# Kernel optimization log

Measured on AMD Instinct MI355X. Metric: run time of the kernel, lower is better.

The kernel has to match this reference:

```python
import jax, jax.numpy as jnp
import numpy as np

DIM = 1024
HEADS = 16
HEAD_DIM = DIM // HEADS  # 64


def get_rope_matrix(seq_len: int, dim: int) -> jnp.ndarray:
    # rope[s, d] = concat(cos(s * inv_freq), sin(s * inv_freq))  -> (seq_len, dim)
    half = dim // 2
    inv_freq = 1.0 / (10000.0 ** (jnp.arange(half, dtype=jnp.float32) / half))
    sinusoid = jnp.arange(seq_len, dtype=jnp.float32)[:, None] * inv_freq[None, :]
    return jnp.concatenate([jnp.cos(sinusoid), jnp.sin(sinusoid)], axis=-1)


def setup_inputs() -> dict:
    key = jax.random.key(0)
    ks = jax.random.split(key, 6)
    B, T, D = 2, 2048, DIM
    scale = 1.0 / np.sqrt(D)
    return {
        "x": jax.random.normal(ks[0], (B, T, D), dtype=jnp.float32),
        "Wq": jax.random.normal(ks[1], (D, D), dtype=jnp.float32) * scale,
        "Wk": jax.random.normal(ks[2], (D, D), dtype=jnp.float32) * scale,
        "Wv": jax.random.normal(ks[3], (D, D), dtype=jnp.float32) * scale,
        "Wo": jax.random.normal(ks[4], (D, D), dtype=jnp.float32) * scale,
        "bo": jax.random.normal(ks[5], (D,), dtype=jnp.float32) * 0.01,
    }


def reference(x, Wq, Wk, Wv, Wo, bo):
    B, T, D = x.shape
    H, hd = HEADS, HEAD_DIM

    # projections -> (B, H, T, hd)
    def split_heads(y):
        return y.reshape(B, T, H, hd).transpose(0, 2, 1, 3)

    q = split_heads(x @ Wq)
    k = split_heads(x @ Wk)
    v = split_heads(x @ Wv)

    rope = get_rope_matrix(T, hd)  # (T, hd)

    # apply_rope(v, rope): einsum('...nd,sd->...ns') contracts head_dim -> (B,H,T,T)
    v_r = jnp.einsum('bhnd,sd->bhns', v, rope)

    scores = jax.nn.softmax(jnp.einsum('bhnd,bhmd->bhnm', q, k) / jnp.sqrt(jnp.float32(hd)), axis=-1)
    out = jnp.einsum('bhnm,bhms->bhns', scores, v_r)  # (B,H,T,T)

    # apply_rope(out, rope.T): out2[...,n,s] = sum_t out[...,n,t] * rope[t,s] -> (B,H,T,hd)
    out = jnp.einsum('bhnt,ts->bhns', out, rope)

    out = out.transpose(0, 2, 1, 3).reshape(B, T, D)
    return out @ Wo + bo
```

## Files before the change

kernel.cpp:

```cpp
#include <hip/hip_runtime.h>
#include <math.h>

#define DIM 1024
#define NH 16
#define HD 64
#define TT 2048
#define NTOK 4096

typedef __bf16 bf8v __attribute__((ext_vector_type(8)));
typedef float f4v __attribute__((ext_vector_type(4)));
typedef unsigned short us8 __attribute__((ext_vector_type(8)));
typedef unsigned short us4 __attribute__((ext_vector_type(4)));

static __device__ __forceinline__ unsigned short f2bf(float f) {
    unsigned int u = __float_as_uint(f);
    u += 0x7FFFu + ((u >> 16) & 1u);
    return (unsigned short)(u >> 16);
}
static __device__ __forceinline__ bf8v ld8(const unsigned short* p) {
    return __builtin_bit_cast(bf8v, *(const us8*)p);
}
static __device__ __forceinline__ void gl_lds(const unsigned short* g, unsigned short* l) {
    __builtin_amdgcn_global_load_lds((const __attribute__((address_space(1))) unsigned int*)(g),
                                     (__attribute__((address_space(3))) unsigned int*)(l), 16, 0, 0);
}

__global__ void k_prep(const float* __restrict__ x, unsigned short* __restrict__ xb,
                       const float* __restrict__ Wq, const float* __restrict__ Wk,
                       const float* __restrict__ Wv, unsigned short* __restrict__ wt,
                       float* __restrict__ rope) {
    int tid = threadIdx.x;
    int bb = blockIdx.x;
    if (bb < 4096) {
        int i = bb * 256 + tid;
        float4 v = ((const float4*)x)[i];
        us4 o;
        o[0] = f2bf(v.x); o[1] = f2bf(v.y); o[2] = f2bf(v.z); o[3] = f2bf(v.w);
        *(us4*)&xb[i * 4] = o;
    } else if (bb < 7168) {
        __shared__ float tile[32][33];
        bb -= 4096;
        int z = bb >> 10, rem = bb & 1023;
        int bx = rem & 31, by = rem >> 5;
        const float* W = (z == 0) ? Wq : ((z == 1) ? Wk : Wv);
        int tx = tid & 31, ty = tid >> 5;
        int c0 = bx * 32, k0 = by * 32;
#pragma unroll
        for (int j = 0; j < 4; j++)
            tile[ty + j * 8][tx] = W[(k0 + ty + j * 8) * DIM + c0 + tx];
        __syncthreads();
        unsigned short* out = wt + z * DIM * DIM;
#pragma unroll
        for (int j = 0; j < 4; j++)
            out[(c0 + ty + j * 8) * DIM + k0 + tx] = f2bf(tile[tx][ty + j * 8]);
    } else {
        int i = (bb - 7168) * 256 + tid;
        int s = i >> 6, d = i & 63;
        float inv = exp2f(-(float)(d & 31) * (13.287712379549449f / 32.0f));
        float a = (float)s * inv;
        rope[i] = (d < 32) ? cosf(a) : sinf(a);
    }
}

__global__ void k_R(const float* __restrict__ rope, float* __restrict__ R) {
    __shared__ float red[256];
    int d = blockIdx.x;
    int e = threadIdx.x & 63, sl = threadIdx.x >> 6;
    const float* rp = rope + sl * 512 * 64;
    float acc = 0.f;
    for (int s = 0; s < 512; s++)
        acc += rp[s * 64 + d] * rp[s * 64 + e];
    red[threadIdx.x] = acc;
    __syncthreads();
    if (sl == 0)
        R[d * 64 + e] = (red[e] + red[e + 64]) + (red[e + 128] + red[e + 192]);
}

__global__ void k_wo2(const float* __restrict__ Wo, const float* __restrict__ R,
                      unsigned short* __restrict__ wo2t) {
    __shared__ float Ws[64 * 65];
    __shared__ float Rt[64 * 65];
    int tid = threadIdx.x;
    int h = blockIdx.y, j0 = blockIdx.x * 64;
    for (int idx = tid; idx < 4096; idx += 256) {
        int e = idx >> 6, j = idx & 63;
        Ws[e * 65 + j] = Wo[(h * 64 + e) * DIM + j0 + j];
        Rt[e * 65 + j] = R[j * 64 + e];
    }
    __syncthreads();
    int d = tid & 63, jb = (tid >> 6) * 16;
    float acc[16] = {};
    for (int e = 0; e < 64; e++) {
        float r = Rt[e * 65 + d];
#pragma unroll
        for (int jj = 0; jj < 16; jj++)
            acc[jj] += r * Ws[e * 65 + jb + jj];
    }
#pragma unroll
    for (int jj = 0; jj < 16; jj++)
        wo2t[(j0 + jb + jj) * DIM + h * 64 + d] = f2bf(acc[jj]);
}


__global__ __launch_bounds__(256, 3) void k_gemm_qkv(const unsigned short* __restrict__ A,
                                                     const unsigned short* __restrict__ Bt,
                                                     unsigned short* __restrict__ qk,
                                                     unsigned short* __restrict__ vt) {
    __shared__ unsigned short As[128 * 32];
    __shared__ unsigned short Bs[128 * 32];
    const int K = 1024;
    int tid = threadIdx.x;
    int lane = tid & 63, w = tid >> 6;
    int quad = lane >> 4, l16 = lane & 15;
    int m0 = blockIdx.y * 128, n0 = blockIdx.x * 128;
    int wm = (w >> 1) * 64, wn = (w & 1) * 64;

    int s0 = tid, s1 = 256 + tid;
    int r0 = s0 >> 2, cc0 = ((s0 & 3) ^ (r0 & 3)) * 8;
    int r1 = s1 >> 2, cc1 = ((s1 & 3) ^ (r1 & 3)) * 8;
    const unsigned short* Ag0 = A + (m0 + r0) * K + cc0;
    const unsigned short* Ag1 = A + (m0 + r1) * K + cc1;
    const unsigned short* Bg0 = Bt + (n0 + r0) * K + cc0;
    const unsigned short* Bg1 = Bt + (n0 + r1) * K + cc1;
    int qx = quad ^ (l16 & 3);

    f4v acc[4][4] = {};
    for (int k0 = 0; k0 < K; k0 += 32) {
        __syncthreads();
        gl_lds(Ag0 + k0, &As[s0 * 8]);
        gl_lds(Ag1 + k0, &As[s1 * 8]);
        gl_lds(Bg0 + k0, &Bs[s0 * 8]);
        gl_lds(Bg1 + k0, &Bs[s1 * 8]);
        __syncthreads();
        bf8v af[4], bf[4];
#pragma unroll
        for (int mt = 0; mt < 4; mt++)
            af[mt] = ld8(&As[(wm + mt * 16 + l16) * 32 + qx * 8]);
#pragma unroll
        for (int nt = 0; nt < 4; nt++)
            bf[nt] = ld8(&Bs[(wn + nt * 16 + l16) * 32 + qx * 8]);
#pragma unroll
        for (int mt = 0; mt < 4; mt++)
#pragma unroll
            for (int nt = 0; nt < 4; nt++)
                acc[mt][nt] = __builtin_amdgcn_mfma_f32_16x16x32_bf16(af[mt], bf[nt], acc[mt][nt], 0, 0, 0);
    }
#pragma unroll
    for (int mt = 0; mt < 4; mt++) {
#pragma unroll
        for (int nt = 0; nt < 4; nt++) {
            int gc = n0 + wn + nt * 16 + l16;
            int h = (gc >> 6) & 15;
            int d = gc & 63;
            if (gc < 2048) {
                float qs = (gc < 1024) ? 0.18033688011111793f : 1.0f;
                int mtx = gc >> 10;
                unsigned short* base = qk + mtx * (NTOK * DIM);
#pragma unroll
                for (int r = 0; r < 4; r++) {
                    int gm = m0 + wm + mt * 16 + quad * 4 + r;
                    int b = gm >> 11, t = gm & 2047;
                    base[((b * NH + h) * TT + t) * HD + d] = f2bf(acc[mt][nt][r] * qs);
                }
            } else {
                int gm0 = m0 + wm + mt * 16 + quad * 4;
                int b = gm0 >> 11, t = gm0 & 2047;
                us4 ov;
#pragma unroll
                for (int r = 0; r < 4; r++)
                    ov[r] = f2bf(acc[mt][nt][r]);
                *(us4*)&vt[(((b * NH + h) * HD) + d) * TT + t] = ov;
            }
        }
    }
}

__global__ __launch_bounds__(256, 3) void k_gemm_out(const unsigned short* __restrict__ A,
                                                     const unsigned short* __restrict__ Bt,
                                                     const float* __restrict__ bo,
                                                     float* __restrict__ out) {
    __shared__ unsigned short As[128 * 32];
    __shared__ unsigned short Bs[128 * 32];
    const int K = 1024;
    int tid = threadIdx.x;
    int lane = tid & 63, w = tid >> 6;
    int quad = lane >> 4, l16 = lane & 15;
    int m0 = blockIdx.y * 128, n0 = blockIdx.x * 128;
    int wm = (w >> 1) * 64, wn = (w & 1) * 64;

    int s0 = tid, s1 = 256 + tid;
    int r0 = s0 >> 2, cc0 = ((s0 & 3) ^ (r0 & 3)) * 8;
    int r1 = s1 >> 2, cc1 = ((s1 & 3) ^ (r1 & 3)) * 8;
    const unsigned short* Ag0 = A + (m0 + r0) * K + cc0;
    const unsigned short* Ag1 = A + (m0 + r1) * K + cc1;
    const unsigned short* Bg0 = Bt + (n0 + r0) * K + cc0;
    const unsigned short* Bg1 = Bt + (n0 + r1) * K + cc1;
    int qx = quad ^ (l16 & 3);

    f4v acc[4][4] = {};
    for (int k0 = 0; k0 < K; k0 += 32) {
        __syncthreads();
        gl_lds(Ag0 + k0, &As[s0 * 8]);
        gl_lds(Ag1 + k0, &As[s1 * 8]);
        gl_lds(Bg0 + k0, &Bs[s0 * 8]);
        gl_lds(Bg1 + k0, &Bs[s1 * 8]);
        __syncthreads();
        bf8v af[4], bf[4];
#pragma unroll
        for (int mt = 0; mt < 4; mt++)
            af[mt] = ld8(&As[(wm + mt * 16 + l16) * 32 + qx * 8]);
#pragma unroll
        for (int nt = 0; nt < 4; nt++)
            bf[nt] = ld8(&Bs[(wn + nt * 16 + l16) * 32 + qx * 8]);
#pragma unroll
        for (int mt = 0; mt < 4; mt++)
#pragma unroll
            for (int nt = 0; nt < 4; nt++)
                acc[mt][nt] = __builtin_amdgcn_mfma_f32_16x16x32_bf16(af[mt], bf[nt], acc[mt][nt], 0, 0, 0);
    }
#pragma unroll
    for (int mt = 0; mt < 4; mt++) {
#pragma unroll
        for (int nt = 0; nt < 4; nt++) {
            int gc = n0 + wn + nt * 16 + l16;
            float bias = bo[gc];
#pragma unroll
            for (int r = 0; r < 4; r++) {
                int gm = m0 + wm + mt * 16 + quad * 4 + r;
                out[gm * DIM + gc] = acc[mt][nt][r] + bias;
            }
        }
    }
}

#define LQ 72
__global__ __launch_bounds__(256, 4) void k_flash(const unsigned short* __restrict__ qk,
                                                  const unsigned short* __restrict__ vt,
                                                  unsigned short* __restrict__ Op,
                                                  float* __restrict__ Ls) {
    __shared__ unsigned short Ks[64 * LQ];
    __shared__ unsigned short Vs[80 * LQ];
    __shared__ unsigned short Ps[128 * LQ];
    int tid = threadIdx.x;
    int lane = tid & 63, w = tid >> 6;
    int quad = lane >> 4, l16 = lane & 15;
    int bh = blockIdx.x & 31;
    int sp = (blockIdx.x >> 5) & 1;
    int qt = blockIdx.x >> 6;
    const unsigned short* Qg = qk + bh * (TT * HD);
    const unsigned short* Kg = qk + NTOK * DIM + bh * (TT * HD);
    const unsigned short* Vtg = vt + bh * (HD * TT);

    for (int idx = tid; idx < 16 * LQ; idx += 256)
        Vs[64 * LQ + idx] = (idx < LQ) ? (unsigned short)0x3F80 : (unsigned short)0;

    {
        int r = tid >> 1, c0 = (tid & 1) * 32;
        const us8* src = (const us8*)(Qg + (qt * 128 + r) * HD + c0);
#pragma unroll
        for (int i = 0; i < 4; i++)
            *(us8*)&Ps[r * LQ + c0 + i * 8] = src[i];
    }
    bf8v qf[2][2];
#pragma unroll
    for (int g = 0; g < 2; g++)
#pragma unroll
        for (int ks = 0; ks < 2; ks++)
            qf[g][ks] = ld8(&Ps[(w * 32 + g * 16 + l16) * LQ + ks * 32 + quad * 8]);

    int sr = tid >> 2, sc = (tid & 3) * 16;
    const unsigned short* Kgp = Kg + (sp * 1024 + sr) * HD + sc;
    const unsigned short* Vgp = Vtg + sr * TT + sp * 1024 + sc;
    us8 kr0 = *(const us8*)(Kgp);
    us8 kr1 = *(const us8*)(Kgp + 8);
    us8 vr0 = *(const us8*)(Vgp);
    us8 vr1 = *(const us8*)(Vgp + 8);

    f4v oacc[5][2] = {};

    for (int it = 0; it < 16; it++) {
        __syncthreads();
        *(us8*)&Ks[sr * LQ + sc] = kr0;
        *(us8*)&Ks[sr * LQ + sc + 8] = kr1;
        *(us8*)&Vs[sr * LQ + sc] = vr0;
        *(us8*)&Vs[sr * LQ + sc + 8] = vr1;
        __syncthreads();
        if (it < 15) {
            Kgp += 64 * HD;
            Vgp += 64;
            kr0 = *(const us8*)(Kgp);
            kr1 = *(const us8*)(Kgp + 8);
            vr0 = *(const us8*)(Vgp);
            vr1 = *(const us8*)(Vgp + 8);
        }

        f4v sacc[4][2] = {};
#pragma unroll
        for (int ks = 0; ks < 2; ks++) {
            bf8v kf[4];
#pragma unroll
            for (int mt = 0; mt < 4; mt++)
                kf[mt] = ld8(&Ks[(mt * 16 + l16) * LQ + ks * 32 + quad * 8]);
#pragma unroll
            for (int mt = 0; mt < 4; mt++)
#pragma unroll
                for (int g = 0; g < 2; g++)
                    sacc[mt][g] = __builtin_amdgcn_mfma_f32_16x16x32_bf16(kf[mt], qf[g][ks], sacc[mt][g], 0, 0, 0);
        }

#pragma unroll
        for (int g = 0; g < 2; g++) {
#pragma unroll
            for (int mt = 0; mt < 4; mt++) {
                float p0 = __builtin_amdgcn_exp2f(sacc[mt][g][0]);
                float p1 = __builtin_amdgcn_exp2f(sacc[mt][g][1]);
                float p2 = __builtin_amdgcn_exp2f(sacc[mt][g][2]);
                float p3 = __builtin_amdgcn_exp2f(sacc[mt][g][3]);
                unsigned int d0 = __builtin_amdgcn_perm(__float_as_uint(p1), __float_as_uint(p0), 0x07060302u);
                unsigned int d1 = __builtin_amdgcn_perm(__float_as_uint(p3), __float_as_uint(p2), 0x07060302u);
                uint2 pk; pk.x = d0; pk.y = d1;
                *(uint2*)&Ps[(w * 32 + g * 16 + l16) * LQ + mt * 16 + quad * 4] = pk;
            }
        }

#pragma unroll
        for (int ks = 0; ks < 2; ks++) {
            bf8v pf[2];
#pragma unroll
            for (int g = 0; g < 2; g++)
                pf[g] = ld8(&Ps[(w * 32 + g * 16 + l16) * LQ + ks * 32 + quad * 8]);
#pragma unroll
            for (int mtd = 0; mtd < 5; mtd++) {
                bf8v vf = ld8(&Vs[(mtd * 16 + l16) * LQ + ks * 32 + quad * 8]);
#pragma unroll
                for (int g = 0; g < 2; g++)
                    oacc[mtd][g] = __builtin_amdgcn_mfma_f32_16x16x32_bf16(vf, pf[g], oacc[mtd][g], 0, 0, 0);
            }
        }
    }

    int b = bh >> 4, h = bh & 15;
    unsigned short* Opd = Op + sp * (NTOK * DIM);
#pragma unroll
    for (int g = 0; g < 2; g++) {
        int t = qt * 128 + w * 32 + g * 16 + l16;
        unsigned short* dst = Opd + (b * TT + t) * DIM + h * HD;
#pragma unroll
        for (int mtd = 0; mtd < 4; mtd++) {
            us4 ov;
#pragma unroll
            for (int r = 0; r < 4; r++)
                ov[r] = f2bf(oacc[mtd][g][r]);
            *(us4*)&dst[mtd * 16 + quad * 4] = ov;
        }
        if (quad == 0)
            Ls[sp * 65536 + bh * 2048 + t] = oacc[4][g][0];
    }
}

__global__ void k_comb(const unsigned short* __restrict__ Op, const float* __restrict__ Ls,
                       unsigned short* __restrict__ attn) {
    int e = (blockIdx.x * 256 + threadIdx.x) * 8;
    int h = (e >> 6) & 15, t = (e >> 10) & 2047, b = e >> 21;
    int bh = b * 16 + h;
    float inv = 1.0f / (Ls[bh * 2048 + t] + Ls[65536 + bh * 2048 + t]);
    us8 a = *(const us8*)&Op[e];
    us8 c = *(const us8*)&Op[NTOK * DIM + e];
    us8 o;
#pragma unroll
    for (int j = 0; j < 8; j++) {
        float fa = __uint_as_float((unsigned int)a[j] << 16);
        float fc = __uint_as_float((unsigned int)c[j] << 16);
        o[j] = f2bf((fa + fc) * inv);
    }
    *(us8*)&attn[e] = o;
}

extern "C" void kernel_launch(void* const* d_in, const int* in_sizes, int n_in,
                              void* d_out, int out_size, void* d_ws, size_t ws_size,
                              hipStream_t stream) {
    const float* x  = (const float*)d_in[0];
    const float* Wq = (const float*)d_in[1];
    const float* Wk = (const float*)d_in[2];
    const float* Wv = (const float*)d_in[3];
    const float* Wo = (const float*)d_in[4];
    const float* bo = (const float*)d_in[5];
    float* out = (float*)d_out;
    char* ws = (char*)d_ws;

    unsigned short* Xb    = (unsigned short*)(ws);
    unsigned short* Wqkvt = (unsigned short*)(ws + 8388608);
    unsigned short* Op    = (unsigned short*)(ws);
    unsigned short* QK    = (unsigned short*)(ws + 16777216);
    unsigned short* Vt    = (unsigned short*)(ws + 33554432);
    unsigned short* attn  = (unsigned short*)(ws + 41943040);
    unsigned short* Wo2t  = (unsigned short*)(ws + 50331648);
    float*          rope  = (float*)(ws + 52428800);
    float*          Rm    = (float*)(ws + 52953088);
    float*          Ls    = (float*)(ws + 52969472);

    hipLaunchKernelGGL(k_prep,     dim3(7680),   dim3(256), 0, stream, x, Xb, Wq, Wk, Wv, Wqkvt, rope);
    hipLaunchKernelGGL(k_R,        dim3(64),     dim3(256), 0, stream, rope, Rm);
    hipLaunchKernelGGL(k_wo2,      dim3(16, 16), dim3(256), 0, stream, Wo, Rm, Wo2t);
    hipLaunchKernelGGL(k_gemm_qkv, dim3(24, 32), dim3(256), 0, stream, Xb, Wqkvt, QK, Vt);
    hipLaunchKernelGGL(k_flash,    dim3(1024),   dim3(256), 0, stream, QK, Vt, Op, Ls);
    hipLaunchKernelGGL(k_comb,     dim3(2048),   dim3(256), 0, stream, Op, Ls, attn);
    hipLaunchKernelGGL(k_gemm_out, dim3(8, 32),  dim3(256), 0, stream, attn, Wo2t, bo, out);
}
```

Measured before the change: 220.6 us.

## Rewrite flash kernel with register-resident 32x32 MFMA, no LDS staging

The attention inner kernel switches from 16x16x32 MFMAs with K, V and P staged through shared memory to 32x32x16 MFMAs. K and V fragments are read directly from global memory into registers, and P is repacked in registers with cvt_pk_bf16 and permlane32_swap instead of a round trip through LDS. The softmax row sum is accumulated in registers rather than through an extra ones-row in V. Block indices are remapped so that each XCD works on the same heads, and s_setprio is raised around the MFMA sections. This removes the LDS traffic and barriers, at the cost of uncoalesced or repeated global loads per wave that now depend on L2 reuse.

```diff
diff --git a/kernel.cpp b/kernel.cpp
--- a/kernel.cpp
+++ b/kernel.cpp
@@ -9,8 +9,10 @@
 
 typedef __bf16 bf8v __attribute__((ext_vector_type(8)));
 typedef float f4v __attribute__((ext_vector_type(4)));
+typedef float f16v __attribute__((ext_vector_type(16)));
 typedef unsigned short us8 __attribute__((ext_vector_type(8)));
 typedef unsigned short us4 __attribute__((ext_vector_type(4)));
+typedef unsigned int u4v __attribute__((ext_vector_type(4)));
 
 static __device__ __forceinline__ unsigned short f2bf(float f) {
     unsigned int u = __float_as_uint(f);
@@ -233,129 +235,117 @@
     }
 }
 
-#define LQ 72
 __global__ __launch_bounds__(256, 4) void k_flash(const unsigned short* __restrict__ qk,
                                                   const unsigned short* __restrict__ vt,
                                                   unsigned short* __restrict__ Op,
                                                   float* __restrict__ Ls) {
-    __shared__ unsigned short Ks[64 * LQ];
-    __shared__ unsigned short Vs[80 * LQ];
-    __shared__ unsigned short Ps[128 * LQ];
     int tid = threadIdx.x;
     int lane = tid & 63, w = tid >> 6;
-    int quad = lane >> 4, l16 = lane & 15;
-    int bh = blockIdx.x & 31;
-    int sp = (blockIdx.x >> 5) & 1;
-    int qt = blockIdx.x >> 6;
+    int q31 = lane & 31, hi = lane >> 5;
+    int bid = blockIdx.x;
+    int xcd = bid & 7, slot = bid >> 3;
+    int bh = xcd * 4 + (slot & 3);
+    int sp = (slot >> 2) & 1;
+    int qt = slot >> 3;
+
     const unsigned short* Qg = qk + bh * (TT * HD);
-    const unsigned short* Kg = qk + NTOK * DIM + bh * (TT * HD);
-    const unsigned short* Vtg = vt + bh * (HD * TT);
-
-    for (int idx = tid; idx < 16 * LQ; idx += 256)
-        Vs[64 * LQ + idx] = (idx < LQ) ? (unsigned short)0x3F80 : (unsigned short)0;
-
-    {
-        int r = tid >> 1, c0 = (tid & 1) * 32;
-        const us8* src = (const us8*)(Qg + (qt * 128 + r) * HD + c0);
-#pragma unroll
-        for (int i = 0; i < 4; i++)
-            *(us8*)&Ps[r * LQ + c0 + i * 8] = src[i];
-    }
-    bf8v qf[2][2];
-#pragma unroll
-    for (int g = 0; g < 2; g++)
-#pragma unroll
-        for (int ks = 0; ks < 2; ks++)
-            qf[g][ks] = ld8(&Ps[(w * 32 + g * 16 + l16) * LQ + ks * 32 + quad * 8]);
-
-    int sr = tid >> 2, sc = (tid & 3) * 16;
-    const unsigned short* Kgp = Kg + (sp * 1024 + sr) * HD + sc;
-    const unsigned short* Vgp = Vtg + sr * TT + sp * 1024 + sc;
-    us8 kr0 = *(const us8*)(Kgp);
-    us8 kr1 = *(const us8*)(Kgp + 8);
-    us8 vr0 = *(const us8*)(Vgp);
-    us8 vr1 = *(const us8*)(Vgp + 8);
-
-    f4v oacc[5][2] = {};
+    const unsigned short* Kg = qk + NTOK * DIM + bh * (TT * HD) + sp * 1024 * HD;
+    const unsigned short* Vg = vt + bh * (HD * TT) + sp * 1024;
+
+    int qrow = qt * 128 + w * 32 + q31;
+    bf8v qf[4];
+#pragma unroll
+    for (int ks = 0; ks < 4; ks++)
+        qf[ks] = ld8(Qg + qrow * HD + ks * 16 + hi * 8);
+
+    const unsigned short* Kp = Kg + q31 * HD + hi * 8;
+    const unsigned short* Vp = Vg + q31 * TT + hi * 8;
+
+    f16v oacc[2] = {};
+    float ls = 0.f;
 
     for (int it = 0; it < 16; it++) {
-        __syncthreads();
-        *(us8*)&Ks[sr * LQ + sc] = kr0;
-        *(us8*)&Ks[sr * LQ + sc + 8] = kr1;
-        *(us8*)&Vs[sr * LQ + sc] = vr0;
-        *(us8*)&Vs[sr * LQ + sc + 8] = vr1;
-        __syncthreads();
-        if (it < 15) {
-            Kgp += 64 * HD;
-            Vgp += 64;
-            kr0 = *(const us8*)(Kgp);
-            kr1 = *(const us8*)(Kgp + 8);
-            vr0 = *(const us8*)(Vgp);
-            vr1 = *(const us8*)(Vgp + 8);
-        }
-
-        f4v sacc[4][2] = {};
-#pragma unroll
-        for (int ks = 0; ks < 2; ks++) {
+        int kb = it * 64;
+        f16v s0 = {}, s1 = {};
+        {
             bf8v kf[4];
 #pragma unroll
-            for (int mt = 0; mt < 4; mt++)
-                kf[mt] = ld8(&Ks[(mt * 16 + l16) * LQ + ks * 32 + quad * 8]);
-#pragma unroll
-            for (int mt = 0; mt < 4; mt++)
-#pragma unroll
-                for (int g = 0; g < 2; g++)
-                    sacc[mt][g] = __builtin_amdgcn_mfma_f32_16x16x32_bf16(kf[mt], qf[g][ks], sacc[mt][g], 0, 0, 0);
-        }
-
-#pragma unroll
-        for (int g = 0; g < 2; g++) {
-#pragma unroll
-            for (int mt = 0; mt < 4; mt++) {
-                float p0 = __builtin_amdgcn_exp2f(sacc[mt][g][0]);
-                float p1 = __builtin_amdgcn_exp2f(sacc[mt][g][1]);
-                float p2 = __builtin_amdgcn_exp2f(sacc[mt][g][2]);
-                float p3 = __builtin_amdgcn_exp2f(sacc[mt][g][3]);
-                unsigned int d0 = __builtin_amdgcn_perm(__float_as_uint(p1), __float_as_uint(p0), 0x07060302u);
-                unsigned int d1 = __builtin_amdgcn_perm(__float_as_uint(p3), __float_as_uint(p2), 0x07060302u);
-                uint2 pk; pk.x = d0; pk.y = d1;
-                *(uint2*)&Ps[(w * 32 + g * 16 + l16) * LQ + mt * 16 + quad * 4] = pk;
+            for (int ks = 0; ks < 4; ks++)
+                kf[ks] = ld8(Kp + kb * HD + ks * 16);
+            __builtin_amdgcn_s_setprio(1);
+#pragma unroll
+            for (int ks = 0; ks < 4; ks++)
+                s0 = __builtin_amdgcn_mfma_f32_32x32x16_bf16(kf[ks], qf[ks], s0, 0, 0, 0);
+            __builtin_amdgcn_s_setprio(0);
+        }
+        {
+            bf8v kf[4];
+#pragma unroll
+            for (int ks = 0; ks < 4; ks++)
+                kf[ks] = ld8(Kp + (kb + 32) * HD + ks * 16);
+            __builtin_amdgcn_s_setprio(1);
+#pragma unroll
+            for (int ks = 0; ks < 4; ks++)
+                s1 = __builtin_amdgcn_mfma_f32_32x32x16_bf16(kf[ks], qf[ks], s1, 0, 0, 0);
+            __builtin_amdgcn_s_setprio(0);
+        }
+
+        bf8v vf[2][4];
+#pragma unroll
+        for (int kk = 0; kk < 4; kk++)
+#pragma unroll
+            for (int mtd = 0; mtd < 2; mtd++)
+                vf[mtd][kk] = ld8(Vp + mtd * 32 * TT + kb + kk * 16);
+
+        bf8v pb[4];
+#pragma unroll
+        for (int mt = 0; mt < 2; mt++) {
+            f16v s = mt ? s1 : s0;
+#pragma unroll
+            for (int sub = 0; sub < 2; sub++) {
+                float pe[8];
+#pragma unroll
+                for (int j = 0; j < 8; j++) {
+                    pe[j] = __builtin_amdgcn_exp2f(s[sub * 8 + j]);
+                    ls += pe[j];
+                }
+                unsigned int d0, d1, d2, d3;
+                asm("v_cvt_pk_bf16_f32 %0, %1, %2" : "=v"(d0) : "v"(pe[0]), "v"(pe[1]));
+                asm("v_cvt_pk_bf16_f32 %0, %1, %2" : "=v"(d1) : "v"(pe[2]), "v"(pe[3]));
+                asm("v_cvt_pk_bf16_f32 %0, %1, %2" : "=v"(d2) : "v"(pe[4]), "v"(pe[5]));
+                asm("v_cvt_pk_bf16_f32 %0, %1, %2" : "=v"(d3) : "v"(pe[6]), "v"(pe[7]));
+                asm("v_permlane32_swap_b32 %0, %1" : "+v"(d0), "+v"(d2));
+                asm("v_permlane32_swap_b32 %0, %1" : "+v"(d1), "+v"(d3));
+                u4v pv = {d0, d1, d2, d3};
+                pb[mt * 2 + sub] = __builtin_bit_cast(bf8v, pv);
             }
         }
 
-#pragma unroll
-        for (int ks = 0; ks < 2; ks++) {
-            bf8v pf[2];
-#pragma unroll
-            for (int g = 0; g < 2; g++)
-                pf[g] = ld8(&Ps[(w * 32 + g * 16 + l16) * LQ + ks * 32 + quad * 8]);
-#pragma unroll
-            for (int mtd = 0; mtd < 5; mtd++) {
-                bf8v vf = ld8(&Vs[(mtd * 16 + l16) * LQ + ks * 32 + quad * 8]);
-#pragma unroll
-                for (int g = 0; g < 2; g++)
-                    oacc[mtd][g] = __builtin_amdgcn_mfma_f32_16x16x32_bf16(vf, pf[g], oacc[mtd][g], 0, 0, 0);
-            }
-        }
-    }
-
+        __builtin_amdgcn_s_setprio(1);
+#pragma unroll
+        for (int kk = 0; kk < 4; kk++)
+#pragma unroll
+            for (int mtd = 0; mtd < 2; mtd++)
+                oacc[mtd] = __builtin_amdgcn_mfma_f32_32x32x16_bf16(vf[mtd][kk], pb[kk], oacc[mtd], 0, 0, 0);
+        __builtin_amdgcn_s_setprio(0);
+    }
+
+    float lsum = ls + __shfl_xor(ls, 32, 64);
     int b = bh >> 4, h = bh & 15;
-    unsigned short* Opd = Op + sp * (NTOK * DIM);
-#pragma unroll
-    for (int g = 0; g < 2; g++) {
-        int t = qt * 128 + w * 32 + g * 16 + l16;
-        unsigned short* dst = Opd + (b * TT + t) * DIM + h * HD;
-#pragma unroll
-        for (int mtd = 0; mtd < 4; mtd++) {
+    unsigned short* dst = Op + sp * (NTOK * DIM) + ((b * TT) + qrow) * DIM + h * HD + hi * 4;
+#pragma unroll
+    for (int mtd = 0; mtd < 2; mtd++) {
+#pragma unroll
+        for (int g = 0; g < 4; g++) {
             us4 ov;
 #pragma unroll
             for (int r = 0; r < 4; r++)
-                ov[r] = f2bf(oacc[mtd][g][r]);
-            *(us4*)&dst[mtd * 16 + quad * 4] = ov;
-        }
-        if (quad == 0)
-            Ls[sp * 65536 + bh * 2048 + t] = oacc[4][g][0];
-    }
+                ov[r] = f2bf(oacc[mtd][g * 4 + r]);
+            *(us4*)&dst[mtd * 32 + g * 8] = ov;
+        }
+    }
+    if (hi == 0)
+        Ls[sp * 65536 + bh * 2048 + qrow] = lsum;
 }
 
 __global__ void k_comb(const unsigned short* __restrict__ Op, const float* __restrict__ Ls,
```

New measurement: 295.2 us. +33.8%, slower.
